# Optimization experiments

Measured on AMD Instinct MI355X. Metric: run time of the kernel, lower is better.

Reference implementation:

```python
import jax, jax.numpy as jnp
import numpy as np

T = 0.07  # temperature
EPS = 1e-12

MEM, DIM = 262144, 128
BS, NPOS, NNEG = 256, 8, 1024


def _l2norm(x):
    # torch F.normalize(p=2, dim=1): x / max(||x||, eps)
    n = jnp.sqrt(jnp.sum(x * x, axis=-1, keepdims=True))
    return x / jnp.maximum(n, EPS)


def setup_inputs() -> dict:
    key = jax.random.key(0)
    k = jax.random.split(key, 7)
    return {
        "video_emb": jax.random.normal(k[0], (BS, DIM), jnp.float32),
        "audio_emb": jax.random.normal(k[1], (BS, DIM), jnp.float32),
        "view1_mem": _l2norm(jax.random.normal(k[2], (MEM, DIM), jnp.float32)),
        "view2_mem": _l2norm(jax.random.normal(k[3], (MEM, DIM), jnp.float32)),
        "y": jax.random.randint(k[4], (BS,), 0, MEM, jnp.int32),
        "pos_idx": jax.random.randint(k[5], (BS, NPOS), 0, MEM, jnp.int32),
        "neg_idx": jax.random.randint(k[6], (BS, NNEG), 0, MEM, jnp.int32),
    }


def reference(video_emb, audio_emb, view1_mem, view2_mem, y, pos_idx, neg_idx):
    # normalize query embeddings (xModal=True, wModal=False path)
    v = _l2norm(video_emb)  # (bs, d)
    a = _l2norm(audio_emb)  # (bs, d)

    # no-grad memory gathers
    v_self = view1_mem[y][:, None, :]   # (bs, 1, d)
    a_self = view2_mem[y][:, None, :]
    v_pos = view1_mem[pos_idx]          # (bs, P, d)
    a_pos = view2_mem[pos_idx]
    v_neg = view1_mem[neg_idx]          # (bs, N, d)
    a_neg = view2_mem[neg_idx]

    # xModal scores: targets dotted with context embedding, scaled by 1/T
    xm_a = jnp.concatenate([a_self, a_pos, a_neg], axis=1)  # (bs, 1+P+N, d)
    xm_v = jnp.concatenate([v_self, v_pos, v_neg], axis=1)
    v2a = jnp.einsum('bkd,bd->bk', xm_a, v) / T  # (bs, 1+P+N)
    a2v = jnp.einsum('bkd,bd->bk', xm_v, a) / T
    return jnp.stack([v2a, a2v], axis=0)  # (2, bs, 1+P+N)
```

## Files before the change

### kernel.cpp

```cpp
#include <hip/hip_runtime.h>

#define MEMN 262144
#define DIM 128
#define BS 256
#define NPOS 8
#define NNEG 1024
#define KTOT (1 + NPOS + NNEG)
#define NCHUNK 8
#define CHUNKK ((KTOT + NCHUNK - 1) / NCHUNK)

__global__ __launch_bounds__(256) void avid_sim_kernel(
    const float* __restrict__ video, const float* __restrict__ audio,
    const float* __restrict__ view1, const float* __restrict__ view2,
    const int* __restrict__ y, const int* __restrict__ pos,
    const int* __restrict__ neg, float* __restrict__ out)
{
    const int bid   = blockIdx.x;
    const int m     = bid / (BS * NCHUNK);
    const int rem   = bid - m * (BS * NCHUNK);
    const int b     = rem / NCHUNK;
    const int chunk = rem - b * NCHUNK;

    const float* q_src = (m == 0) ? (video + b * DIM) : (audio + b * DIM);
    const float* mem   = (m == 0) ? view2 : view1;

    const int g   = threadIdx.x & 15;
    const int grp = threadIdx.x >> 4;

    float4 q0 = *(const float4*)(q_src + g * 8);
    float4 q1 = *(const float4*)(q_src + g * 8 + 4);

    float qq = q0.x*q0.x + q0.y*q0.y + q0.z*q0.z + q0.w*q0.w
             + q1.x*q1.x + q1.y*q1.y + q1.z*q1.z + q1.w*q1.w;
    qq += __shfl_xor(qq, 1);
    qq += __shfl_xor(qq, 2);
    qq += __shfl_xor(qq, 4);
    qq += __shfl_xor(qq, 8);
    const float scale = (1.0f / 0.07f) / fmaxf(sqrtf(qq), 1e-12f);
    q0.x *= scale; q0.y *= scale; q0.z *= scale; q0.w *= scale;
    q1.x *= scale; q1.y *= scale; q1.z *= scale; q1.w *= scale;

    float* outm = out + (size_t)m * BS * KTOT + (size_t)b * KTOT;

    const int k0 = chunk * CHUNKK;
    const int k1 = (k0 + CHUNKK < KTOT) ? (k0 + CHUNKK) : KTOT;

    for (int k = k0 + grp; k < k1; k += 16) {
        int idx;
        if (k == 0)          idx = y[b];
        else if (k <= NPOS)  idx = pos[b * NPOS + (k - 1)];
        else                 idx = neg[b * NNEG + (k - 1 - NPOS)];

        const float* row = mem + (size_t)idx * DIM;
        float4 r0 = *(const float4*)(row + g * 8);
        float4 r1 = *(const float4*)(row + g * 8 + 4);

        float s = q0.x*r0.x + q0.y*r0.y + q0.z*r0.z + q0.w*r0.w
                + q1.x*r1.x + q1.y*r1.y + q1.z*r1.z + q1.w*r1.w;
        s += __shfl_xor(s, 1);
        s += __shfl_xor(s, 2);
        s += __shfl_xor(s, 4);
        s += __shfl_xor(s, 8);
        if (g == 0) outm[k] = s;
    }
}

extern "C" void kernel_launch(void* const* d_in, const int* in_sizes, int n_in,
                              void* d_out, int out_size, void* d_ws, size_t ws_size,
                              hipStream_t stream) {
    const float* video = (const float*)d_in[0];
    const float* audio = (const float*)d_in[1];
    const float* view1 = (const float*)d_in[2];
    const float* view2 = (const float*)d_in[3];
    const int*   y     = (const int*)d_in[4];
    const int*   pos   = (const int*)d_in[5];
    const int*   neg   = (const int*)d_in[6];
    float* out = (float*)d_out;

    dim3 grid(2 * BS * NCHUNK);
    dim3 block(256);
    avid_sim_kernel<<<grid, block, 0, stream>>>(video, audio, view1, view2,
                                                y, pos, neg, out);
}
```

Before: 45.07 us.

## Bucket gather indices by memory row and compute both modalities per bucket

Splits the work into three kernels. The first pre-normalizes the queries into a workspace. The second scatters every (b, k) gather index into 2048 buckets keyed by memory row range, using atomics. The third processes each bucket, reading view1 and view2 rows for both modalities in one pass so that repeated and nearby rows are served from cache rather than DRAM. In exchange it adds two extra launches, contended atomics, and indirect output writes. A fixed bucket capacity of 320 silently drops entries if the indices are not roughly uniform.

```diff
diff --git a/kernel.cpp b/kernel.cpp
--- a/kernel.cpp
+++ b/kernel.cpp
@@ -5,63 +5,116 @@
 #define BS 256
 #define NPOS 8
 #define NNEG 1024
-#define KTOT (1 + NPOS + NNEG)
-#define NCHUNK 8
-#define CHUNKK ((KTOT + NCHUNK - 1) / NCHUNK)
+#define KTOT 1033
+#define NK (BS * KTOT)
+#define NBKT 2048
+#define BSHIFT 7
+#define CAP 320
+#define CSTRIDE 16
+#define TSCALE 14.285714285714286f
 
-__global__ __launch_bounds__(256) void avid_sim_kernel(
+#define COUNTS_OFF 262144
+#define ENTRIES_OFF 393216
+
+__global__ __launch_bounds__(256) void prep_kernel(
     const float* __restrict__ video, const float* __restrict__ audio,
-    const float* __restrict__ view1, const float* __restrict__ view2,
-    const int* __restrict__ y, const int* __restrict__ pos,
-    const int* __restrict__ neg, float* __restrict__ out)
+    float* __restrict__ qbuf, int* __restrict__ counts)
 {
-    const int bid   = blockIdx.x;
-    const int m     = bid / (BS * NCHUNK);
-    const int rem   = bid - m * (BS * NCHUNK);
-    const int b     = rem / NCHUNK;
-    const int chunk = rem - b * NCHUNK;
+    const int t = blockIdx.x * 256 + threadIdx.x;
+    if (t < NBKT) counts[t << 4] = 0;
 
-    const float* q_src = (m == 0) ? (video + b * DIM) : (audio + b * DIM);
-    const float* mem   = (m == 0) ? view2 : view1;
+    const int row = t >> 4;
+    const int g   = t & 15;
+    const int m   = row >> 8;
+    const int b   = row & 255;
+    const float* src = (m ? audio : video) + b * DIM + g * 8;
 
-    const int g   = threadIdx.x & 15;
-    const int grp = threadIdx.x >> 4;
-
-    float4 q0 = *(const float4*)(q_src + g * 8);
-    float4 q1 = *(const float4*)(q_src + g * 8 + 4);
-
+    float4 q0 = *(const float4*)(src);
+    float4 q1 = *(const float4*)(src + 4);
     float qq = q0.x*q0.x + q0.y*q0.y + q0.z*q0.z + q0.w*q0.w
              + q1.x*q1.x + q1.y*q1.y + q1.z*q1.z + q1.w*q1.w;
     qq += __shfl_xor(qq, 1);
     qq += __shfl_xor(qq, 2);
     qq += __shfl_xor(qq, 4);
     qq += __shfl_xor(qq, 8);
-    const float scale = (1.0f / 0.07f) / fmaxf(sqrtf(qq), 1e-12f);
+    const float scale = TSCALE / fmaxf(sqrtf(qq), 1e-12f);
     q0.x *= scale; q0.y *= scale; q0.z *= scale; q0.w *= scale;
     q1.x *= scale; q1.y *= scale; q1.z *= scale; q1.w *= scale;
 
-    float* outm = out + (size_t)m * BS * KTOT + (size_t)b * KTOT;
+    float* dst = qbuf + (size_t)row * DIM + g * 8;
+    *(float4*)(dst)     = q0;
+    *(float4*)(dst + 4) = q1;
+}
 
-    const int k0 = chunk * CHUNKK;
-    const int k1 = (k0 + CHUNKK < KTOT) ? (k0 + CHUNKK) : KTOT;
-
-    for (int k = k0 + grp; k < k1; k += 16) {
+__global__ __launch_bounds__(256) void scatter_kernel(
+    const int* __restrict__ y, const int* __restrict__ pos,
+    const int* __restrict__ neg, int* __restrict__ counts,
+    uint2* __restrict__ entries)
+{
+    const int b = blockIdx.x;
+    for (int k = threadIdx.x; k < KTOT; k += 256) {
         int idx;
         if (k == 0)          idx = y[b];
         else if (k <= NPOS)  idx = pos[b * NPOS + (k - 1)];
         else                 idx = neg[b * NNEG + (k - 1 - NPOS)];
+        const int bkt = idx >> BSHIFT;
+        const int slot = atomicAdd(&counts[bkt << 4], 1);
+        if (slot < CAP)
+            entries[bkt * CAP + slot] = make_uint2((unsigned)idx,
+                                                   ((unsigned)b << 11) | (unsigned)k);
+    }
+}
 
-        const float* row = mem + (size_t)idx * DIM;
-        float4 r0 = *(const float4*)(row + g * 8);
-        float4 r1 = *(const float4*)(row + g * 8 + 4);
+__global__ __launch_bounds__(256) void compute_kernel(
+    const float* __restrict__ view1, const float* __restrict__ view2,
+    const float* __restrict__ qbuf, const int* __restrict__ counts,
+    const uint2* __restrict__ entries, float* __restrict__ out)
+{
+    const int bkt = blockIdx.x;
+    int cnt = counts[bkt << 4];
+    if (cnt > CAP) cnt = CAP;
+    const int g   = threadIdx.x & 15;
+    const int grp = threadIdx.x >> 4;
+    const uint2* ebase = entries + (size_t)bkt * CAP;
 
-        float s = q0.x*r0.x + q0.y*r0.y + q0.z*r0.z + q0.w*r0.w
-                + q1.x*r1.x + q1.y*r1.y + q1.z*r1.z + q1.w*r1.w;
-        s += __shfl_xor(s, 1);
-        s += __shfl_xor(s, 2);
-        s += __shfl_xor(s, 4);
-        s += __shfl_xor(s, 8);
-        if (g == 0) outm[k] = s;
+    for (int i = grp; i < cnt; i += 16) {
+        const uint2 e = ebase[i];
+        const int idx = (int)e.x;
+        const int b   = (int)(e.y >> 11);
+        const int k   = (int)(e.y & 2047u);
+
+        const float* r2 = view2 + (size_t)idx * DIM + g * 8;
+        const float* r1 = view1 + (size_t)idx * DIM + g * 8;
+        const float* qv = qbuf + (size_t)b * DIM + g * 8;
+        const float* qa = qbuf + (size_t)(BS + b) * DIM + g * 8;
+
+        float4 a0 = *(const float4*)(r2);
+        float4 a1 = *(const float4*)(r2 + 4);
+        float4 b0 = *(const float4*)(r1);
+        float4 b1 = *(const float4*)(r1 + 4);
+        float4 v0 = *(const float4*)(qv);
+        float4 v1 = *(const float4*)(qv + 4);
+        float4 u0 = *(const float4*)(qa);
+        float4 u1 = *(const float4*)(qa + 4);
+
+        float s0 = a0.x*v0.x + a0.y*v0.y + a0.z*v0.z + a0.w*v0.w
+                 + a1.x*v1.x + a1.y*v1.y + a1.z*v1.z + a1.w*v1.w;
+        float s1 = b0.x*u0.x + b0.y*u0.y + b0.z*u0.z + b0.w*u0.w
+                 + b1.x*u1.x + b1.y*u1.y + b1.z*u1.z + b1.w*u1.w;
+
+        s0 += __shfl_xor(s0, 1);
+        s0 += __shfl_xor(s0, 2);
+        s0 += __shfl_xor(s0, 4);
+        s0 += __shfl_xor(s0, 8);
+        s1 += __shfl_xor(s1, 1);
+        s1 += __shfl_xor(s1, 2);
+        s1 += __shfl_xor(s1, 4);
+        s1 += __shfl_xor(s1, 8);
+
+        if (g == 0) {
+            out[(size_t)b * KTOT + k] = s0;
+            out[(size_t)BS * KTOT + (size_t)b * KTOT + k] = s1;
+        }
     }
 }
 
@@ -77,8 +130,12 @@
     const int*   neg   = (const int*)d_in[6];
     float* out = (float*)d_out;
 
-    dim3 grid(2 * BS * NCHUNK);
-    dim3 block(256);
-    avid_sim_kernel<<<grid, block, 0, stream>>>(video, audio, view1, view2,
-                                                y, pos, neg, out);
+    char* ws = (char*)d_ws;
+    float* qbuf    = (float*)ws;
+    int*   counts  = (int*)(ws + COUNTS_OFF);
+    uint2* entries = (uint2*)(ws + ENTRIES_OFF);
+
+    prep_kernel<<<32, 256, 0, stream>>>(video, audio, qbuf, counts);
+    scatter_kernel<<<BS, 256, 0, stream>>>(y, pos, neg, counts, entries);
+    compute_kernel<<<NBKT, 256, 0, stream>>>(view1, view2, qbuf, counts, entries, out);
 }
```

Result: slower. 72.27 us (+60.4%).
